# Kernel tuning notes

Hardware: AMD Instinct MI355X
Metric: run time of the kernel (lower is better)

The kernel has to match this reference:

```python
import jax, jax.numpy as jnp
import numpy as np


def to_float8(x, exp_bits=4, mant_bits=3):
    # Faithful port of the torch to_float8: clamp exponent, round mantissa.
    max_exp = 2 ** (exp_bits - 1) - 1
    scale = 2.0 ** mant_bits
    sign = jnp.sign(x)
    xa = jnp.abs(x)
    e = jnp.clip(jnp.floor(jnp.log2(xa + 1e-08)), -max_exp, max_exp)
    p = jnp.exp2(e)
    mant_q = jnp.round((xa / p - 1.0) * scale) / scale
    return sign * (1.0 + mant_q) * p


def setup_inputs() -> dict:
    key = jax.random.key(0)
    k0, k1, k2, k3, k4 = jax.random.split(key, 5)
    Bz, Din, L, N, Dout = 32, 512, 512, 512, 512
    u = jax.random.normal(k0, (Bz, Din, L), jnp.float32)
    # |A| < 1 for a stable length-512 recurrence
    A_diag = jax.random.uniform(k1, (N,), jnp.float32, 0.0, 0.9)
    B = jax.random.normal(k2, (N, Din), jnp.float32) * (1.0 / np.sqrt(Din))
    C = jax.random.normal(k3, (Dout, N), jnp.float32) * (1.0 / np.sqrt(N))
    D = jax.random.normal(k4, (Dout, Din), jnp.float32) * (1.0 / np.sqrt(Din))
    return {"u": u, "A_diag": A_diag, "B": B, "C": C, "D": D}


def reference(u, A_diag, B, C, D):
    int_bits, mant_bits = 4, 3
    q = lambda t: to_float8(t, int_bits, mant_bits)
    A_q = q(A_diag)[None, :]          # [1, N]
    B_q, C_q, D_q = q(B), q(C), q(D)
    Bt = B_q.T                         # [Din, N]
    # row_checksum(B_q.t()): append column of row sums -> constant across steps
    right_cs = jnp.concatenate([Bt, Bt.sum(axis=1, keepdims=True)], axis=1)  # [Din, N+1]
    Bz, Din, L = u.shape
    N = A_diag.shape[0]
    u_t = jnp.transpose(u, (2, 0, 1))  # [L, Bz, Din]

    def step(state, ut):
        # col_checksum(ut): append row of column sums
        left_cs = jnp.concatenate([ut, ut.sum(axis=0, keepdims=True)], axis=0)  # [Bz+1, Din]
        prod_cs = left_cs @ right_cs                 # [Bz+1, N+1] checksum-padded matmul
        right_term = prod_cs[:-1, :-1]               # ut @ B_q.T  (ABFT mask is discarded in forward)
        state_q = q(state * A_q + right_term)        # [Bz, N]
        y = q(state_q @ C_q.T + ut @ D_q.T)          # [Bz, Dout]
        return state_q, y

    state0 = jnp.zeros((Bz, N), u.dtype)
    _, Y = jax.lax.scan(step, state0, u_t)           # [L, Bz, Dout]
    return jnp.transpose(Y, (1, 2, 0))               # [Bz, Dout, L]
```

## Files before the change

### kernel.cpp

```cpp
#include <hip/hip_runtime.h>
#include <hip/hip_bf16.h>


#define DINX 512
#define LSEQ 512
#define NDIM 512

__device__ __forceinline__ float q8(float x) {
    float xa = fabsf(x);
    float w  = __fadd_rn(xa, 1e-8f);
    int e = (int)((__float_as_uint(w) >> 23) & 0xFFu) - 127;
    e = e < -7 ? -7 : (e > 7 ? 7 : e);
    float p  = __int_as_float((unsigned)((e + 127) << 23));
    float t  = __fmul_rn(__fsub_rn(__fdiv_rn(xa, p), 1.0f), 8.0f);
    float m  = __fmul_rn(rintf(t), 0.125f);
    float r  = __fmul_rn(__fadd_rn(1.0f, m), p);
    return copysignf(r, x);
}

__global__ void quantk(const float* __restrict__ in, float* __restrict__ out, int n) {
    int i = blockIdx.x * blockDim.x + threadIdx.x;
    if (i < n) out[i] = q8(in[i]);
}

__global__ __launch_bounds__(256) void quantT(const float* __restrict__ in,
                                              float* __restrict__ out) {
    __shared__ float tl[32][33];
    const int r0 = blockIdx.y * 32, c0 = blockIdx.x * 32;
    const int x = threadIdx.x & 31, y = threadIdx.x >> 5;
#pragma unroll
    for (int i = 0; i < 32; i += 8)
        tl[y + i][x] = q8(in[(r0 + y + i) * 512 + c0 + x]);
    __syncthreads();
#pragma unroll
    for (int i = 0; i < 32; i += 8)
        out[(c0 + y + i) * 512 + r0 + x] = tl[x][y + i];
}

__device__ __forceinline__ void gemm_pass(const float* __restrict__ X,
                                          const float* __restrict__ W,
                                          int m0, int n0, int KTOT,
                                          float (&acc)[8][8],
                                          float (*Xs)[128], float (*Ws)[128],
                                          int tid) {
    const int tx = tid & 15, ty = tid >> 4;
    const int srow = tid >> 4;
    const int sseg = tid & 15;
    for (int k0 = 0; k0 < KTOT; k0 += 16) {
        const float* xp = X + (size_t)(k0 + srow) * 512 + m0 + sseg * 8;
        const float* wp = W + (size_t)(k0 + srow) * 512 + n0 + sseg * 8;
        float4 x0 = *(const float4*)xp;
        float4 x1 = *(const float4*)(xp + 4);
        float4 w0 = *(const float4*)wp;
        float4 w1 = *(const float4*)(wp + 4);
        __syncthreads();
        *(float4*)&Xs[srow][sseg * 8]     = x0;
        *(float4*)&Xs[srow][sseg * 8 + 4] = x1;
        *(float4*)&Ws[srow][sseg * 8]     = w0;
        *(float4*)&Ws[srow][sseg * 8 + 4] = w1;
        __syncthreads();
#pragma unroll
        for (int k = 0; k < 16; ++k) {
            float a[8], b[8];
            *(float4*)&a[0] = *(const float4*)&Xs[k][tx * 8];
            *(float4*)&a[4] = *(const float4*)&Xs[k][tx * 8 + 4];
            *(float4*)&b[0] = *(const float4*)&Ws[k][ty * 8];
            *(float4*)&b[4] = *(const float4*)&Ws[k][ty * 8 + 4];
#pragma unroll
            for (int i = 0; i < 8; ++i)
#pragma unroll
                for (int j = 0; j < 8; ++j)
                    acc[i][j] = fmaf(a[i], b[j], acc[i][j]);
        }
    }
}

__global__ __launch_bounds__(256) void gemm_R(const float* __restrict__ u,
                                              const float* __restrict__ Bqt,
                                              float* __restrict__ R) {
    __shared__ float Xs[16][128];
    __shared__ float Ws[16][128];
    const int b  = blockIdx.z;
    const int t0 = blockIdx.x * 128, n0 = blockIdx.y * 128;
    const int tid = threadIdx.x;
    const int tx = tid & 15, ty = tid >> 4;
    const float* ub = u + (size_t)b * (DINX * LSEQ);
    float acc[8][8] = {};
    gemm_pass(ub, Bqt, t0, n0, DINX, acc, Xs, Ws, tid);
    float* Rb = R + (size_t)b * (LSEQ * NDIM);
#pragma unroll
    for (int i = 0; i < 8; ++i) {
        float* row = Rb + (size_t)(t0 + tx * 8 + i) * NDIM + n0 + ty * 8;
        *(float4*)row       = make_float4(acc[i][0], acc[i][1], acc[i][2], acc[i][3]);
        *(float4*)(row + 4) = make_float4(acc[i][4], acc[i][5], acc[i][6], acc[i][7]);
    }
}

__global__ __launch_bounds__(512) void recur(const float* __restrict__ R,
                                             const float* __restrict__ Aq,
                                             float* __restrict__ S) {
    __shared__ float tile[16][516];
    const int b = blockIdx.x;
    const int n = threadIdx.x;
    const float a = Aq[n];
    const float* Rb = R + (size_t)b * (LSEQ * NDIM);
    float* Sb = S + (size_t)b * (NDIM * LSEQ);
    float s = 0.0f;
    const int c = (n & 3) * 4;
    const int rbase = n >> 2;
    for (int t0 = 0; t0 < LSEQ; t0 += 16) {
#pragma unroll
        for (int tt = 0; tt < 16; ++tt) {
            float r = Rb[(t0 + tt) * NDIM + n];
            s = q8(__fadd_rn(__fmul_rn(s, a), r));
            tile[tt][n] = s;
        }
        __syncthreads();
#pragma unroll
        for (int p = 0; p < 4; ++p) {
            int row = p * 128 + rbase;
            float4 v = make_float4(tile[c + 0][row], tile[c + 1][row],
                                   tile[c + 2][row], tile[c + 3][row]);
            *(float4*)(Sb + row * LSEQ + t0 + c) = v;
        }
        __syncthreads();
    }
}

__global__ __launch_bounds__(256) void gemm_Y(const float* __restrict__ u,
                                              const float* __restrict__ S,
                                              const float* __restrict__ Cqt,
                                              const float* __restrict__ Dqt,
                                              float* __restrict__ Y) {
    __shared__ float Xs[16][128];
    __shared__ float Ws[16][128];
    const int b  = blockIdx.z;
    const int t0 = blockIdx.x * 128, o0 = blockIdx.y * 128;
    const int tid = threadIdx.x;
    const int tx = tid & 15, ty = tid >> 4;
    const float* Sb = S + (size_t)b * (NDIM * LSEQ);
    const float* ub = u + (size_t)b * (DINX * LSEQ);
    float acc[8][8] = {};
    float c1[8][8];
    gemm_pass(Sb, Cqt, t0, o0, NDIM, acc, Xs, Ws, tid);
#pragma unroll
    for (int i = 0; i < 8; ++i)
#pragma unroll
        for (int j = 0; j < 8; ++j) { c1[i][j] = acc[i][j]; acc[i][j] = 0.0f; }
    __syncthreads();
    gemm_pass(ub, Dqt, t0, o0, DINX, acc, Xs, Ws, tid);

    float* Yb = Y + (size_t)b * (NDIM * LSEQ);
#pragma unroll
    for (int j = 0; j < 8; ++j) {
        float y0[4], y1[4];
#pragma unroll
        for (int i = 0; i < 4; ++i) y0[i] = q8(__fadd_rn(c1[i][j], acc[i][j]));
#pragma unroll
        for (int i = 0; i < 4; ++i) y1[i] = q8(__fadd_rn(c1[4 + i][j], acc[4 + i][j]));
        float* row = Yb + (size_t)(o0 + ty * 8 + j) * LSEQ + t0 + tx * 8;
        *(float4*)row       = make_float4(y0[0], y0[1], y0[2], y0[3]);
        *(float4*)(row + 4) = make_float4(y1[0], y1[1], y1[2], y1[3]);
    }
}

extern "C" void kernel_launch(void* const* d_in, const int* in_sizes, int n_in,
                              void* d_out, int out_size, void* d_ws, size_t ws_size,
                              hipStream_t stream) {
    const float* u = (const float*)d_in[0];
    const float* A = (const float*)d_in[1];
    const float* B = (const float*)d_in[2];
    const float* C = (const float*)d_in[3];
    const float* D = (const float*)d_in[4];

    float* ws  = (float*)d_ws;
    float* Aq  = ws;
    float* Bqt = Aq + 512;
    float* Cqt = Bqt + 262144;
    float* Dqt = Cqt + 262144;
    float* R   = Dqt + 262144;
    float* S   = R + 8388608;
    float* Y   = (float*)d_out;

    quantk<<<2, 256, 0, stream>>>(A, Aq, 512);
    quantT<<<dim3(16, 16), 256, 0, stream>>>(B, Bqt);
    quantT<<<dim3(16, 16), 256, 0, stream>>>(C, Cqt);
    quantT<<<dim3(16, 16), 256, 0, stream>>>(D, Dqt);

    gemm_R<<<dim3(4, 4, 32), 256, 0, stream>>>(u, Bqt, R);
    recur<<<32, 512, 0, stream>>>(R, Aq, S);
    gemm_Y<<<dim3(4, 4, 32), 256, 0, stream>>>(u, S, Cqt, Dqt, Y);
}
```

Baseline: 450.1 us.

## Split recurrence across more blocks, double-buffer GEMMs, fuse quant kernels, drop division

The recurrence kernel now splits the state dimension across four blocks per batch, giving 128 blocks instead of 32, so more compute units share the serial scan. Both GEMM kernels now double-buffer shared memory and prefetch the next tile into registers, which halves the barriers per k-step. gemm_Y also drops the barrier between its two passes. The three weight-quantize launches become one launch, and q8 multiplies by an exact reciprocal power of two instead of dividing. The larger shared footprint could lower GEMM occupancy, and removing the inter-pass barrier relies on the buffer alternation being race-free.

```diff
diff --git a/kernel.cpp b/kernel.cpp
--- a/kernel.cpp
+++ b/kernel.cpp
@@ -11,8 +11,9 @@
     float w  = __fadd_rn(xa, 1e-8f);
     int e = (int)((__float_as_uint(w) >> 23) & 0xFFu) - 127;
     e = e < -7 ? -7 : (e > 7 ? 7 : e);
-    float p  = __int_as_float((unsigned)((e + 127) << 23));
-    float t  = __fmul_rn(__fsub_rn(__fdiv_rn(xa, p), 1.0f), 8.0f);
+    float p    = __int_as_float((unsigned)((e + 127) << 23));
+    float invp = __int_as_float((unsigned)((127 - e) << 23));
+    float t  = __fmul_rn(__fsub_rn(__fmul_rn(xa, invp), 1.0f), 8.0f);
     float m  = __fmul_rn(rintf(t), 0.125f);
     float r  = __fmul_rn(__fadd_rn(1.0f, m), p);
     return copysignf(r, x);
@@ -23,9 +24,15 @@
     if (i < n) out[i] = q8(in[i]);
 }
 
-__global__ __launch_bounds__(256) void quantT(const float* __restrict__ in,
-                                              float* __restrict__ out) {
+__global__ __launch_bounds__(256) void quantT3(const float* __restrict__ B,
+                                               const float* __restrict__ C,
+                                               const float* __restrict__ D,
+                                               float* __restrict__ Bqt,
+                                               float* __restrict__ Cqt,
+                                               float* __restrict__ Dqt) {
     __shared__ float tl[32][33];
+    const float* in = blockIdx.z == 0 ? B : (blockIdx.z == 1 ? C : D);
+    float* out      = blockIdx.z == 0 ? Bqt : (blockIdx.z == 1 ? Cqt : Dqt);
     const int r0 = blockIdx.y * 32, c0 = blockIdx.x * 32;
     const int x = threadIdx.x & 31, y = threadIdx.x >> 5;
 #pragma unroll
@@ -35,51 +42,77 @@
 #pragma unroll
     for (int i = 0; i < 32; i += 8)
         out[(c0 + y + i) * 512 + r0 + x] = tl[x][y + i];
+}
+
+template <int CUR>
+__device__ __forceinline__ void gemm_step(const float* __restrict__ xp,
+                                          const float* __restrict__ wp,
+                                          int k0, int KTOT,
+                                          float4& x0, float4& x1, float4& w0, float4& w1,
+                                          float (&acc)[8][8],
+                                          float (*Xs)[16][128], float (*Ws)[16][128],
+                                          int srow, int sseg8, int tx, int ty) {
+    __syncthreads();
+    if (k0 + 16 < KTOT) {
+        *(float4*)&Xs[1 - CUR][srow][sseg8]     = x0;
+        *(float4*)&Xs[1 - CUR][srow][sseg8 + 4] = x1;
+        *(float4*)&Ws[1 - CUR][srow][sseg8]     = w0;
+        *(float4*)&Ws[1 - CUR][srow][sseg8 + 4] = w1;
+    }
+    if (k0 + 32 < KTOT) {
+        const float* xn = xp + (size_t)(k0 + 32) * 512;
+        const float* wn = wp + (size_t)(k0 + 32) * 512;
+        x0 = *(const float4*)xn; x1 = *(const float4*)(xn + 4);
+        w0 = *(const float4*)wn; w1 = *(const float4*)(wn + 4);
+    }
+#pragma unroll
+    for (int k = 0; k < 16; ++k) {
+        float a[8], b[8];
+        *(float4*)&a[0] = *(const float4*)&Xs[CUR][k][tx * 8];
+        *(float4*)&a[4] = *(const float4*)&Xs[CUR][k][tx * 8 + 4];
+        *(float4*)&b[0] = *(const float4*)&Ws[CUR][k][ty * 8];
+        *(float4*)&b[4] = *(const float4*)&Ws[CUR][k][ty * 8 + 4];
+#pragma unroll
+        for (int i = 0; i < 8; ++i)
+#pragma unroll
+            for (int j = 0; j < 8; ++j)
+                acc[i][j] = fmaf(a[i], b[j], acc[i][j]);
+    }
 }
 
 __device__ __forceinline__ void gemm_pass(const float* __restrict__ X,
                                           const float* __restrict__ W,
                                           int m0, int n0, int KTOT,
                                           float (&acc)[8][8],
-                                          float (*Xs)[128], float (*Ws)[128],
+                                          float (*Xs)[16][128], float (*Ws)[16][128],
                                           int tid) {
     const int tx = tid & 15, ty = tid >> 4;
-    const int srow = tid >> 4;
-    const int sseg = tid & 15;
-    for (int k0 = 0; k0 < KTOT; k0 += 16) {
-        const float* xp = X + (size_t)(k0 + srow) * 512 + m0 + sseg * 8;
-        const float* wp = W + (size_t)(k0 + srow) * 512 + n0 + sseg * 8;
-        float4 x0 = *(const float4*)xp;
-        float4 x1 = *(const float4*)(xp + 4);
-        float4 w0 = *(const float4*)wp;
-        float4 w1 = *(const float4*)(wp + 4);
-        __syncthreads();
-        *(float4*)&Xs[srow][sseg * 8]     = x0;
-        *(float4*)&Xs[srow][sseg * 8 + 4] = x1;
-        *(float4*)&Ws[srow][sseg * 8]     = w0;
-        *(float4*)&Ws[srow][sseg * 8 + 4] = w1;
-        __syncthreads();
-#pragma unroll
-        for (int k = 0; k < 16; ++k) {
-            float a[8], b[8];
-            *(float4*)&a[0] = *(const float4*)&Xs[k][tx * 8];
-            *(float4*)&a[4] = *(const float4*)&Xs[k][tx * 8 + 4];
-            *(float4*)&b[0] = *(const float4*)&Ws[k][ty * 8];
-            *(float4*)&b[4] = *(const float4*)&Ws[k][ty * 8 + 4];
-#pragma unroll
-            for (int i = 0; i < 8; ++i)
-#pragma unroll
-                for (int j = 0; j < 8; ++j)
-                    acc[i][j] = fmaf(a[i], b[j], acc[i][j]);
-        }
+    const int srow = tid >> 4, sseg8 = (tid & 15) * 8;
+    const float* xp = X + (size_t)srow * 512 + m0 + sseg8;
+    const float* wp = W + (size_t)srow * 512 + n0 + sseg8;
+    float4 x0 = *(const float4*)xp, x1 = *(const float4*)(xp + 4);
+    float4 w0 = *(const float4*)wp, w1 = *(const float4*)(wp + 4);
+    *(float4*)&Xs[0][srow][sseg8]     = x0;
+    *(float4*)&Xs[0][srow][sseg8 + 4] = x1;
+    *(float4*)&Ws[0][srow][sseg8]     = w0;
+    *(float4*)&Ws[0][srow][sseg8 + 4] = w1;
+    {
+        const float* xn = xp + 16 * 512;
+        const float* wn = wp + 16 * 512;
+        x0 = *(const float4*)xn; x1 = *(const float4*)(xn + 4);
+        w0 = *(const float4*)wn; w1 = *(const float4*)(wn + 4);
+    }
+    for (int k0 = 0; k0 < KTOT; k0 += 32) {
+        gemm_step<0>(xp, wp, k0,      KTOT, x0, x1, w0, w1, acc, Xs, Ws, srow, sseg8, tx, ty);
+        gemm_step<1>(xp, wp, k0 + 16, KTOT, x0, x1, w0, w1, acc, Xs, Ws, srow, sseg8, tx, ty);
     }
 }
 
 __global__ __launch_bounds__(256) void gemm_R(const float* __restrict__ u,
                                               const float* __restrict__ Bqt,
                                               float* __restrict__ R) {
-    __shared__ float Xs[16][128];
-    __shared__ float Ws[16][128];
+    __shared__ float Xs[2][16][128];
+    __shared__ float Ws[2][16][128];
     const int b  = blockIdx.z;
     const int t0 = blockIdx.x * 128, n0 = blockIdx.y * 128;
     const int tid = threadIdx.x;
@@ -96,32 +129,33 @@
     }
 }
 
-__global__ __launch_bounds__(512) void recur(const float* __restrict__ R,
+__global__ __launch_bounds__(128) void recur(const float* __restrict__ R,
                                              const float* __restrict__ Aq,
                                              float* __restrict__ S) {
-    __shared__ float tile[16][516];
-    const int b = blockIdx.x;
-    const int n = threadIdx.x;
-    const float a = Aq[n];
-    const float* Rb = R + (size_t)b * (LSEQ * NDIM);
-    float* Sb = S + (size_t)b * (NDIM * LSEQ);
+    __shared__ float tile[16][132];
+    const int b  = blockIdx.x;
+    const int n0 = blockIdx.y * 128;
+    const int n  = threadIdx.x;
+    const float a = Aq[n0 + n];
+    const float* Rb = R + (size_t)b * (LSEQ * NDIM) + n0;
+    float* Sb = S + (size_t)b * (NDIM * LSEQ) + (size_t)n0 * LSEQ;
     float s = 0.0f;
     const int c = (n & 3) * 4;
     const int rbase = n >> 2;
     for (int t0 = 0; t0 < LSEQ; t0 += 16) {
 #pragma unroll
         for (int tt = 0; tt < 16; ++tt) {
-            float r = Rb[(t0 + tt) * NDIM + n];
+            float r = Rb[(size_t)(t0 + tt) * NDIM + n];
             s = q8(__fadd_rn(__fmul_rn(s, a), r));
             tile[tt][n] = s;
         }
         __syncthreads();
 #pragma unroll
         for (int p = 0; p < 4; ++p) {
-            int row = p * 128 + rbase;
+            int row = p * 32 + rbase;
             float4 v = make_float4(tile[c + 0][row], tile[c + 1][row],
                                    tile[c + 2][row], tile[c + 3][row]);
-            *(float4*)(Sb + row * LSEQ + t0 + c) = v;
+            *(float4*)(Sb + (size_t)row * LSEQ + t0 + c) = v;
         }
         __syncthreads();
     }
@@ -132,8 +166,8 @@
                                               const float* __restrict__ Cqt,
                                               const float* __restrict__ Dqt,
                                               float* __restrict__ Y) {
-    __shared__ float Xs[16][128];
-    __shared__ float Ws[16][128];
+    __shared__ float Xs[2][16][128];
+    __shared__ float Ws[2][16][128];
     const int b  = blockIdx.z;
     const int t0 = blockIdx.x * 128, o0 = blockIdx.y * 128;
     const int tid = threadIdx.x;
@@ -147,7 +181,6 @@
     for (int i = 0; i < 8; ++i)
 #pragma unroll
         for (int j = 0; j < 8; ++j) { c1[i][j] = acc[i][j]; acc[i][j] = 0.0f; }
-    __syncthreads();
     gemm_pass(ub, Dqt, t0, o0, DINX, acc, Xs, Ws, tid);
 
     float* Yb = Y + (size_t)b * (NDIM * LSEQ);
@@ -183,11 +216,9 @@
     float* Y   = (float*)d_out;
 
     quantk<<<2, 256, 0, stream>>>(A, Aq, 512);
-    quantT<<<dim3(16, 16), 256, 0, stream>>>(B, Bqt);
-    quantT<<<dim3(16, 16), 256, 0, stream>>>(C, Cqt);
-    quantT<<<dim3(16, 16), 256, 0, stream>>>(D, Dqt);
+    quantT3<<<dim3(16, 16, 3), 256, 0, stream>>>(B, C, D, Bqt, Cqt, Dqt);
 
     gemm_R<<<dim3(4, 4, 32), 256, 0, stream>>>(u, Bqt, R);
-    recur<<<32, 512, 0, stream>>>(R, Aq, S);
+    recur<<<dim3(32, 4), 128, 0, stream>>>(R, Aq, S);
     gemm_Y<<<dim3(4, 4, 32), 256, 0, stream>>>(u, S, Cqt, Dqt, Y);
 }
```

Measured after the change: 529.0 us. 1.18x slower.

## Restructure GEMMs with wave-uniform weight loads and transpose-free recurrence layout

Applied to the files above, without the earlier changes.

The GEMMs now give each wave a 16-column slice of weights read through wave-uniform (scalar) loads, with only the activation tile staged in shared memory. Each thread computes a 2x16 tile, and blocks shrink to 64 output columns to double the grid. R is written transposed ([n][t]), so the recurrence runs 128-thread blocks across a 32x4 grid and each thread streams its own row with float4 loads and stores, with no shared-memory transpose. The division in q8 becomes a multiply by an exact power-of-two reciprocal, and the three weight-quantize launches merge into one. The risks are lower per-thread arithmetic intensity and strided per-thread float4 accesses in the recurrence, which may coalesce poorly.

```diff
diff --git a/kernel.cpp b/kernel.cpp
--- a/kernel.cpp
+++ b/kernel.cpp
@@ -2,17 +2,16 @@
 #include <hip/hip_bf16.h>
 
 
-#define DINX 512
-#define LSEQ 512
-#define NDIM 512
+#define FULL 512
 
 __device__ __forceinline__ float q8(float x) {
     float xa = fabsf(x);
     float w  = __fadd_rn(xa, 1e-8f);
     int e = (int)((__float_as_uint(w) >> 23) & 0xFFu) - 127;
     e = e < -7 ? -7 : (e > 7 ? 7 : e);
-    float p  = __int_as_float((unsigned)((e + 127) << 23));
-    float t  = __fmul_rn(__fsub_rn(__fdiv_rn(xa, p), 1.0f), 8.0f);
+    float p    = __int_as_float((unsigned)((e + 127) << 23));
+    float invp = __int_as_float((unsigned)((127 - e) << 23));
+    float t  = __fmul_rn(__fsub_rn(__fmul_rn(xa, invp), 1.0f), 8.0f);
     float m  = __fmul_rn(rintf(t), 0.125f);
     float r  = __fmul_rn(__fadd_rn(1.0f, m), p);
     return copysignf(r, x);
@@ -23,144 +22,118 @@
     if (i < n) out[i] = q8(in[i]);
 }
 
-__global__ __launch_bounds__(256) void quantT(const float* __restrict__ in,
-                                              float* __restrict__ out) {
+__global__ __launch_bounds__(256) void quantT3(const float* __restrict__ B,
+                                               const float* __restrict__ C,
+                                               const float* __restrict__ D,
+                                               float* __restrict__ Bqt,
+                                               float* __restrict__ Cqt,
+                                               float* __restrict__ Dqt) {
     __shared__ float tl[32][33];
+    const float* in = blockIdx.z == 0 ? B : (blockIdx.z == 1 ? C : D);
+    float* out      = blockIdx.z == 0 ? Bqt : (blockIdx.z == 1 ? Cqt : Dqt);
     const int r0 = blockIdx.y * 32, c0 = blockIdx.x * 32;
     const int x = threadIdx.x & 31, y = threadIdx.x >> 5;
 #pragma unroll
     for (int i = 0; i < 32; i += 8)
-        tl[y + i][x] = q8(in[(r0 + y + i) * 512 + c0 + x]);
+        tl[y + i][x] = q8(in[(r0 + y + i) * FULL + c0 + x]);
     __syncthreads();
 #pragma unroll
     for (int i = 0; i < 32; i += 8)
-        out[(c0 + y + i) * 512 + r0 + x] = tl[x][y + i];
+        out[(c0 + y + i) * FULL + r0 + x] = tl[x][y + i];
 }
 
-__device__ __forceinline__ void gemm_pass(const float* __restrict__ X,
-                                          const float* __restrict__ W,
-                                          int m0, int n0, int KTOT,
-                                          float (&acc)[8][8],
-                                          float (*Xs)[128], float (*Ws)[128],
-                                          int tid) {
-    const int tx = tid & 15, ty = tid >> 4;
-    const int srow = tid >> 4;
-    const int sseg = tid & 15;
-    for (int k0 = 0; k0 < KTOT; k0 += 16) {
-        const float* xp = X + (size_t)(k0 + srow) * 512 + m0 + sseg * 8;
-        const float* wp = W + (size_t)(k0 + srow) * 512 + n0 + sseg * 8;
-        float4 x0 = *(const float4*)xp;
+__device__ __forceinline__ void gemm_pass_sgpr(const float* __restrict__ X,
+                                               const float* __restrict__ Wt,
+                                               int m0, int nw0,
+                                               float (&acc0)[16], float (&acc1)[16],
+                                               float (*Xs)[128],
+                                               int tid, int lane) {
+    const int row = tid >> 4, col = (tid & 15) * 8;
+    const float* xp = X + (size_t)row * FULL + m0 + col;
+    for (int k0 = 0; k0 < FULL; k0 += 16) {
+        float4 x0 = *(const float4*)(xp);
         float4 x1 = *(const float4*)(xp + 4);
-        float4 w0 = *(const float4*)wp;
-        float4 w1 = *(const float4*)(wp + 4);
+        xp += 16 * FULL;
         __syncthreads();
-        *(float4*)&Xs[srow][sseg * 8]     = x0;
-        *(float4*)&Xs[srow][sseg * 8 + 4] = x1;
-        *(float4*)&Ws[srow][sseg * 8]     = w0;
-        *(float4*)&Ws[srow][sseg * 8 + 4] = w1;
+        *(float4*)&Xs[row][col]     = x0;
+        *(float4*)&Xs[row][col + 4] = x1;
         __syncthreads();
+        const float* wb = Wt + (size_t)k0 * FULL + nw0;
 #pragma unroll
         for (int k = 0; k < 16; ++k) {
-            float a[8], b[8];
-            *(float4*)&a[0] = *(const float4*)&Xs[k][tx * 8];
-            *(float4*)&a[4] = *(const float4*)&Xs[k][tx * 8 + 4];
-            *(float4*)&b[0] = *(const float4*)&Ws[k][ty * 8];
-            *(float4*)&b[4] = *(const float4*)&Ws[k][ty * 8 + 4];
+            float2 a = *(const float2*)&Xs[k][lane * 2];
+            const float* wr = wb + (size_t)k * FULL;
 #pragma unroll
-            for (int i = 0; i < 8; ++i)
-#pragma unroll
-                for (int j = 0; j < 8; ++j)
-                    acc[i][j] = fmaf(a[i], b[j], acc[i][j]);
+            for (int j = 0; j < 16; ++j) {
+                float w = wr[j];
+                acc0[j] = fmaf(a.x, w, acc0[j]);
+                acc1[j] = fmaf(a.y, w, acc1[j]);
+            }
         }
     }
 }
 
-__global__ __launch_bounds__(256) void gemm_R(const float* __restrict__ u,
-                                              const float* __restrict__ Bqt,
-                                              float* __restrict__ R) {
+__global__ __launch_bounds__(256, 4) void gemm_R(const float* __restrict__ u,
+                                                 const float* __restrict__ Bqt,
+                                                 float* __restrict__ Rp) {
     __shared__ float Xs[16][128];
-    __shared__ float Ws[16][128];
     const int b  = blockIdx.z;
-    const int t0 = blockIdx.x * 128, n0 = blockIdx.y * 128;
-    const int tid = threadIdx.x;
-    const int tx = tid & 15, ty = tid >> 4;
-    const float* ub = u + (size_t)b * (DINX * LSEQ);
-    float acc[8][8] = {};
-    gemm_pass(ub, Bqt, t0, n0, DINX, acc, Xs, Ws, tid);
-    float* Rb = R + (size_t)b * (LSEQ * NDIM);
+    const int t0 = blockIdx.x * 128, n0 = blockIdx.y * 64;
+    const int tid = threadIdx.x, lane = tid & 63;
+    const int wave = __builtin_amdgcn_readfirstlane(tid >> 6);
+    const int nw0 = n0 + wave * 16;
+    float acc0[16] = {}, acc1[16] = {};
+    gemm_pass_sgpr(u + (size_t)b * (FULL * FULL), Bqt, t0, nw0, acc0, acc1, Xs, tid, lane);
+    float* Rb = Rp + (size_t)b * (FULL * FULL);
 #pragma unroll
-    for (int i = 0; i < 8; ++i) {
-        float* row = Rb + (size_t)(t0 + tx * 8 + i) * NDIM + n0 + ty * 8;
-        *(float4*)row       = make_float4(acc[i][0], acc[i][1], acc[i][2], acc[i][3]);
-        *(float4*)(row + 4) = make_float4(acc[i][4], acc[i][5], acc[i][6], acc[i][7]);
+    for (int j = 0; j < 16; ++j) {
+        float2 v = make_float2(acc0[j], acc1[j]);
+        *(float2*)(Rb + (size_t)(nw0 + j) * FULL + t0 + lane * 2) = v;
     }
 }
 
-__global__ __launch_bounds__(512) void recur(const float* __restrict__ R,
+__global__ __launch_bounds__(128) void recur(const float* __restrict__ Rp,
                                              const float* __restrict__ Aq,
                                              float* __restrict__ S) {
-    __shared__ float tile[16][516];
     const int b = blockIdx.x;
-    const int n = threadIdx.x;
+    const int n = blockIdx.y * 128 + threadIdx.x;
     const float a = Aq[n];
-    const float* Rb = R + (size_t)b * (LSEQ * NDIM);
-    float* Sb = S + (size_t)b * (NDIM * LSEQ);
-    float s = 0.0f;
-    const int c = (n & 3) * 4;
-    const int rbase = n >> 2;
-    for (int t0 = 0; t0 < LSEQ; t0 += 16) {
-#pragma unroll
-        for (int tt = 0; tt < 16; ++tt) {
-            float r = Rb[(t0 + tt) * NDIM + n];
-            s = q8(__fadd_rn(__fmul_rn(s, a), r));
-            tile[tt][n] = s;
-        }
-        __syncthreads();
-#pragma unroll
-        for (int p = 0; p < 4; ++p) {
-            int row = p * 128 + rbase;
-            float4 v = make_float4(tile[c + 0][row], tile[c + 1][row],
-                                   tile[c + 2][row], tile[c + 3][row]);
-            *(float4*)(Sb + row * LSEQ + t0 + c) = v;
-        }
-        __syncthreads();
+    const float* r = Rp + (size_t)b * (FULL * FULL) + (size_t)n * FULL;
+    float* s = S + (size_t)b * (FULL * FULL) + (size_t)n * FULL;
+    float st = 0.0f;
+    for (int t = 0; t < FULL; t += 4) {
+        float4 rv = *(const float4*)(r + t);
+        float4 ov;
+        st = q8(__fadd_rn(__fmul_rn(st, a), rv.x)); ov.x = st;
+        st = q8(__fadd_rn(__fmul_rn(st, a), rv.y)); ov.y = st;
+        st = q8(__fadd_rn(__fmul_rn(st, a), rv.z)); ov.z = st;
+        st = q8(__fadd_rn(__fmul_rn(st, a), rv.w)); ov.w = st;
+        *(float4*)(s + t) = ov;
     }
 }
 
-__global__ __launch_bounds__(256) void gemm_Y(const float* __restrict__ u,
-                                              const float* __restrict__ S,
-                                              const float* __restrict__ Cqt,
-                                              const float* __restrict__ Dqt,
-                                              float* __restrict__ Y) {
+__global__ __launch_bounds__(256, 4) void gemm_Y(const float* __restrict__ u,
+                                                 const float* __restrict__ S,
+                                                 const float* __restrict__ Cqt,
+                                                 const float* __restrict__ Dqt,
+                                                 float* __restrict__ Y) {
     __shared__ float Xs[16][128];
-    __shared__ float Ws[16][128];
     const int b  = blockIdx.z;
-    const int t0 = blockIdx.x * 128, o0 = blockIdx.y * 128;
-    const int tid = threadIdx.x;
-    const int tx = tid & 15, ty = tid >> 4;
-    const float* Sb = S + (size_t)b * (NDIM * LSEQ);
-    const float* ub = u + (size_t)b * (DINX * LSEQ);
-    float acc[8][8] = {};
-    float c1[8][8];
-    gemm_pass(Sb, Cqt, t0, o0, NDIM, acc, Xs, Ws, tid);
+    const int t0 = blockIdx.x * 128, o0 = blockIdx.y * 64;
+    const int tid = threadIdx.x, lane = tid & 63;
+    const int wave = __builtin_amdgcn_readfirstlane(tid >> 6);
+    const int ow0 = o0 + wave * 16;
+    float c0[16] = {}, c1[16] = {};
+    gemm_pass_sgpr(S + (size_t)b * (FULL * FULL), Cqt, t0, ow0, c0, c1, Xs, tid, lane);
+    float a0[16] = {}, a1[16] = {};
+    gemm_pass_sgpr(u + (size_t)b * (FULL * FULL), Dqt, t0, ow0, a0, a1, Xs, tid, lane);
+    float* Yb = Y + (size_t)b * (FULL * FULL);
 #pragma unroll
-    for (int i = 0; i < 8; ++i)
-#pragma unroll
-        for (int j = 0; j < 8; ++j) { c1[i][j] = acc[i][j]; acc[i][j] = 0.0f; }
-    __syncthreads();
-    gemm_pass(ub, Dqt, t0, o0, DINX, acc, Xs, Ws, tid);
-
-    float* Yb = Y + (size_t)b * (NDIM * LSEQ);
-#pragma unroll
-    for (int j = 0; j < 8; ++j) {
-        float y0[4], y1[4];
-#pragma unroll
-        for (int i = 0; i < 4; ++i) y0[i] = q8(__fadd_rn(c1[i][j], acc[i][j]));
-#pragma unroll
-        for (int i = 0; i < 4; ++i) y1[i] = q8(__fadd_rn(c1[4 + i][j], acc[4 + i][j]));
-        float* row = Yb + (size_t)(o0 + ty * 8 + j) * LSEQ + t0 + tx * 8;
-        *(float4*)row       = make_float4(y0[0], y0[1], y0[2], y0[3]);
-        *(float4*)(row + 4) = make_float4(y1[0], y1[1], y1[2], y1[3]);
+    for (int j = 0; j < 16; ++j) {
+        float2 v;
+        v.x = q8(__fadd_rn(c0[j], a0[j]));
+        v.y = q8(__fadd_rn(c1[j], a1[j]));
+        *(float2*)(Yb + (size_t)(ow0 + j) * FULL + t0 + lane * 2) = v;
     }
 }
 
@@ -178,16 +151,14 @@
     float* Bqt = Aq + 512;
     float* Cqt = Bqt + 262144;
     float* Dqt = Cqt + 262144;
-    float* R   = Dqt + 262144;
-    float* S   = R + 8388608;
+    float* Rp  = Dqt + 262144;
+    float* S   = Rp + 8388608;
     float* Y   = (float*)d_out;
 
     quantk<<<2, 256, 0, stream>>>(A, Aq, 512);
-    quantT<<<dim3(16, 16), 256, 0, stream>>>(B, Bqt);
-    quantT<<<dim3(16, 16), 256, 0, stream>>>(C, Cqt);
-    quantT<<<dim3(16, 16), 256, 0, stream>>>(D, Dqt);
+    quantT3<<<dim3(16, 16, 3), 256, 0, stream>>>(B, C, D, Bqt, Cqt, Dqt);
 
-    gemm_R<<<dim3(4, 4, 32), 256, 0, stream>>>(u, Bqt, R);
-    recur<<<32, 512, 0, stream>>>(R, Aq, S);
-    gemm_Y<<<dim3(4, 4, 32), 256, 0, stream>>>(u, S, Cqt, Dqt, Y);
+    gemm_R<<<dim3(4, 8, 32), 256, 0, stream>>>(u, Bqt, Rp);
+    recur<<<dim3(32, 4), 128, 0, stream>>>(Rp, Aq, S);
+    gemm_Y<<<dim3(4, 8, 32), 256, 0, stream>>>(u, S, Cqt, Dqt, Y);
 }
```

Result: slower. 490.9 us (+9.1%).
